# Kernel tuning notes

Measured on AMD Instinct MI355X. Metric: run time of the kernel, lower is better.

Reference implementation:

```python
import jax, jax.numpy as jnp
import numpy as np

N, E, D, C = 100000, 3200000, 256, 47


def _l2norm(x):
    n = jnp.sqrt(jnp.sum(x * x, axis=-1, keepdims=True))
    return x / jnp.maximum(n, 1e-12)


def setup_inputs() -> dict:
    key = jax.random.key(0)
    ks = jax.random.split(key, 12)
    w = lambda k, s: jax.random.normal(k, s, dtype=jnp.float32) * 0.05
    return {
        "x": jax.random.normal(ks[0], (N, D), dtype=jnp.float32),
        "src": jax.random.randint(ks[1], (E,), 0, N, dtype=jnp.int32),
        "dst": jnp.sort(jax.random.randint(ks[2], (E,), 0, N, dtype=jnp.int32)),
        "W_pre": w(ks[3], (D, D)), "b_pre": jnp.zeros((D,), jnp.float32),
        "Wl1": w(ks[4], (D, D)), "bl1": jnp.zeros((D,), jnp.float32),
        "Wr1": w(ks[5], (D, D)),
        "Wl2": w(ks[6], (D, D)), "bl2": jnp.zeros((D,), jnp.float32),
        "Wr2": w(ks[7], (D, D)),
        "W_jk": w(ks[8], (D, D)), "b_jk": jnp.zeros((D,), jnp.float32),
        "W_post": w(ks[9], (C, D)), "b_post": jnp.zeros((C,), jnp.float32),
    }


def _sage_conv(x, src, dst, Wl, bl, Wr):
    # aggr='add': m_i = sum_{j in N(i)} x_j  (SpMM as gather + segment_sum)
    m = jax.ops.segment_sum(x[src], dst, num_segments=N)
    out = m @ Wl.T + bl + x @ Wr.T  # lin_l(aggr) + lin_r(root)
    return _l2norm(out)            # SAGEConv normalize=True


def reference(x, src, dst, W_pre, b_pre, Wl1, bl1, Wr1, Wl2, bl2, Wr2,
              W_jk, b_jk, W_post, b_post):
    # pre-MLP (1 layer) + classifier activation; dropout=0, batch_norm off
    h = jax.nn.relu(x @ W_pre.T + b_pre)
    h = _l2norm(h)  # self.normalize
    # GraphSAGE, jk='last': act+dropout after every conv, then jk lin
    h = jax.nn.relu(_sage_conv(h, src, dst, Wl1, bl1, Wr1))
    h = jax.nn.relu(_sage_conv(h, src, dst, Wl2, bl2, Wr2))
    h = h @ W_jk.T + b_jk
    # post: act + post-MLP (1 layer)
    h = jax.nn.relu(h)
    h = h @ W_post.T + b_post
    return jax.nn.log_softmax(h, axis=-1)
```

## Files before the change

### kernel.cpp

```cpp
#include <hip/hip_runtime.h>
#include <stdint.h>

#define DEV __device__ __forceinline__

typedef __attribute__((ext_vector_type(8))) short bh8;
typedef __attribute__((ext_vector_type(4))) float f4;
#define LDS_AS __attribute__((address_space(3)))
#define GLB_AS __attribute__((address_space(1)))

DEV unsigned short f2bf(float f) {
    union { float f; uint32_t u; } c; c.f = f;
    uint32_t u = c.u;
    uint32_t r = (u + 0x7fffu + ((u >> 16) & 1u)) >> 16;
    return (unsigned short)r;
}
DEV float bf2f(unsigned short h) {
    union { uint32_t u; float f; } c; c.u = ((uint32_t)h) << 16;
    return c.f;
}

DEV uint8_t f2fp8(float v) {
    const float vs = v * 256.f;
    union { float f; uint32_t u; } c; c.f = vs;
    const uint32_t u = c.u + 0x7ffffu + ((c.u >> 20) & 1u);
    const uint32_t f8 = (u >> 20) - 960u;
    return (vs < 0.015625f) ? (uint8_t)0 : (uint8_t)f8;
}
DEV float fp8w(uint32_t x) { union { uint32_t u; float f; } c; c.u = x; return c.f; }

DEV void gload16(const void* g, void* l) {
    __builtin_amdgcn_global_load_lds((const GLB_AS uint32_t*)g, (LDS_AS uint32_t*)l, 16, 0, 0);
}

__global__ __launch_bounds__(256) void prep_kernel(
    const float* __restrict__ x, unsigned short* __restrict__ xb, int n4x, int nbx,
    const float* __restrict__ w0, const float* __restrict__ w1, const float* __restrict__ w2,
    const float* __restrict__ w3, const float* __restrict__ w4, const float* __restrict__ w5,
    unsigned short* __restrict__ wbBase,
    const int* __restrict__ dst, int* __restrict__ rp, int N, int E) {
    const int b = blockIdx.x;
    if (b < nbx) {
        const int i = b * 256 + threadIdx.x;
        if (i < n4x) {
            const float4 v = ((const float4*)x)[i];
            ushort4 o; o.x = f2bf(v.x); o.y = f2bf(v.y); o.z = f2bf(v.z); o.w = f2bf(v.w);
            ((ushort4*)xb)[i] = o;
        }
    } else if (b < nbx + 384) {
        const int wi = (b - nbx) >> 6;
        const int i = ((b - nbx) & 63) * 256 + threadIdx.x;
        const float* s = wi == 0 ? w0 : wi == 1 ? w1 : wi == 2 ? w2 : wi == 3 ? w3 : wi == 4 ? w4 : w5;
        const float4 v = ((const float4*)s)[i];
        ushort4 o; o.x = f2bf(v.x); o.y = f2bf(v.y); o.z = f2bf(v.z); o.w = f2bf(v.w);
        ((ushort4*)(wbBase + (size_t)wi * 65536))[i] = o;
    } else {
        const int i = (b - nbx - 384) * 256 + threadIdx.x;
        if (i <= N) {
            int lo = 0, hi = E;
            while (lo < hi) { int mid = (lo + hi) >> 1; if (dst[mid] < i) lo = mid + 1; else hi = mid; }
            rp[i] = lo;
        }
    }
}

__global__ __launch_bounds__(256) void agg_fp8_kernel(const uint32_t* __restrict__ h32,
                                                      const int* __restrict__ src,
                                                      const int* __restrict__ rp,
                                                      unsigned short* __restrict__ mout, int nNodes) {
    const int node = blockIdx.x * 4 + (threadIdx.x >> 6);
    if (node >= nNodes) return;
    const int lane = threadIdx.x & 63;
    const int beg = __builtin_amdgcn_readfirstlane(rp[node]);
    const int end = __builtin_amdgcn_readfirstlane(rp[node + 1]);
    float a0 = 0.f, a1 = 0.f, a2 = 0.f, a3 = 0.f;
    int e = beg;
    for (; e + 8 <= end; e += 8) {
        int s[8];
#pragma unroll
        for (int i = 0; i < 8; i++) s[i] = src[e + i];
        uint32_t w[8];
#pragma unroll
        for (int i = 0; i < 8; i++) w[i] = h32[(size_t)s[i] * 64 + lane];
#pragma unroll
        for (int i = 0; i < 8; i++) {
            a0 += fp8w((w[i] << 20) & 0x07f00000u);
            a1 += fp8w((w[i] << 12) & 0x07f00000u);
            a2 += fp8w((w[i] << 4)  & 0x07f00000u);
            a3 += fp8w((w[i] >> 4)  & 0x07f00000u);
        }
    }
    for (; e < end; ++e) {
        const uint32_t w = h32[(size_t)src[e] * 64 + lane];
        a0 += fp8w((w << 20) & 0x07f00000u);
        a1 += fp8w((w << 12) & 0x07f00000u);
        a2 += fp8w((w << 4)  & 0x07f00000u);
        a3 += fp8w((w >> 4)  & 0x07f00000u);
    }
    const float sc = 0x1p112f;
    ushort4 o;
    o.x = f2bf(a0 * sc); o.y = f2bf(a1 * sc); o.z = f2bf(a2 * sc); o.w = f2bf(a3 * sc);
    *(ushort4*)&mout[(size_t)node * 256 + (size_t)lane * 4] = o;
}

__global__ __launch_bounds__(256) void agg_kernel(const unsigned short* __restrict__ h,
                                                  const int* __restrict__ src,
                                                  const int* __restrict__ rp,
                                                  unsigned short* __restrict__ mout, int nNodes) {
    const int node = blockIdx.x * 4 + (threadIdx.x >> 6);
    if (node >= nNodes) return;
    const int lane = threadIdx.x & 63;
    const size_t fo = (size_t)lane * 4;
    const int beg = __builtin_amdgcn_readfirstlane(rp[node]);
    const int end = __builtin_amdgcn_readfirstlane(rp[node + 1]);
    float a0 = 0.f, a1 = 0.f, a2 = 0.f, a3 = 0.f;
    int e = beg;
    for (; e + 4 <= end; e += 4) {
        const int s0 = src[e], s1 = src[e+1], s2 = src[e+2], s3 = src[e+3];
        ushort4 v0 = *(const ushort4*)&h[(size_t)s0 * 256 + fo];
        ushort4 v1 = *(const ushort4*)&h[(size_t)s1 * 256 + fo];
        ushort4 v2 = *(const ushort4*)&h[(size_t)s2 * 256 + fo];
        ushort4 v3 = *(const ushort4*)&h[(size_t)s3 * 256 + fo];
        a0 += bf2f(v0.x) + bf2f(v1.x) + bf2f(v2.x) + bf2f(v3.x);
        a1 += bf2f(v0.y) + bf2f(v1.y) + bf2f(v2.y) + bf2f(v3.y);
        a2 += bf2f(v0.z) + bf2f(v1.z) + bf2f(v2.z) + bf2f(v3.z);
        a3 += bf2f(v0.w) + bf2f(v1.w) + bf2f(v2.w) + bf2f(v3.w);
    }
    for (; e < end; ++e) {
        const int s = src[e];
        ushort4 v = *(const ushort4*)&h[(size_t)s * 256 + fo];
        a0 += bf2f(v.x); a1 += bf2f(v.y); a2 += bf2f(v.z); a3 += bf2f(v.w);
    }
    ushort4 o;
    o.x = f2bf(a0); o.y = f2bf(a1); o.z = f2bf(a2); o.w = f2bf(a3);
    *(ushort4*)&mout[(size_t)node * 256 + fo] = o;
}

template <int NSEG, int EPMODE, bool EMIT>
__global__ __launch_bounds__(512) void gemm_kernel(
    const unsigned short* __restrict__ A0, const unsigned short* __restrict__ A1,
    const unsigned short* __restrict__ B0, const unsigned short* __restrict__ B1,
    const float* __restrict__ bias, unsigned short* __restrict__ Out,
    uint8_t* __restrict__ F8, int M) {
    __shared__ unsigned short Alds[2 * 128 * 32];
    __shared__ unsigned short Blds[2 * 256 * 32];
    __shared__ float ssq_lds[8][64];

    const int t = threadIdx.x;
    const int wid = t >> 6;
    const int lane = t & 63;
    const int wr = wid >> 2, wc = wid & 3;
    const int l15 = lane & 15;
    const int kh = lane >> 4;
    const int rowBase = blockIdx.x * 128;

    f4 acc[4][4];
#pragma unroll
    for (int m = 0; m < 4; m++)
#pragma unroll
        for (int n = 0; n < 4; n++) acc[m][n] = f4{0.f, 0.f, 0.f, 0.f};

    const int rA = t >> 2;
    const int sSlotA = (t & 3) ^ ((rA >> 1) & 3);
    int grA = rowBase + rA; if (grA > M - 1) grA = M - 1;
    const size_t gAoff = (size_t)grA * 256 + sSlotA * 8;
    const size_t gBoff0 = (size_t)rA * 256 + sSlotA * 8;
    const size_t gBoff1 = (size_t)(128 + rA) * 256 + sSlotA * 8;

    const int nsteps = NSEG * 8;
    auto STAGE = [&](int s, int buf) {
        const unsigned short* Ap = (NSEG == 2 && s >= 8) ? A1 : A0;
        const unsigned short* Bp = (NSEG == 2 && s >= 8) ? B1 : B0;
        const int k0 = (s & 7) * 32;
        gload16(Ap + gAoff + k0, &Alds[buf * 4096 + wid * 512]);
        gload16(Bp + gBoff0 + k0, &Blds[buf * 8192 + wid * 512]);
        gload16(Bp + gBoff1 + k0, &Blds[buf * 8192 + 4096 + wid * 512]);
    };

    STAGE(0, 0);
    asm volatile("s_waitcnt vmcnt(0)" ::: "memory");
    __syncthreads();

#pragma unroll 2
    for (int s = 0; s < nsteps; ++s) {
        const int cur = s & 1;
        if (s + 1 < nsteps) STAGE(s + 1, cur ^ 1);
        bh8 a[4], b[4];
#pragma unroll
        for (int m = 0; m < 4; m++) {
            const int ra = wr * 64 + m * 16 + l15;
            a[m] = *(const bh8*)&Alds[cur * 4096 + ra * 32 + ((kh ^ ((ra >> 1) & 3)) * 8)];
        }
#pragma unroll
        for (int n = 0; n < 4; n++) {
            const int rb = wc * 64 + n * 16 + l15;
            b[n] = *(const bh8*)&Blds[cur * 8192 + rb * 32 + ((kh ^ ((rb >> 1) & 3)) * 8)];
        }
#pragma unroll
        for (int m = 0; m < 4; m++)
#pragma unroll
            for (int n = 0; n < 4; n++)
                acc[m][n] = __builtin_amdgcn_mfma_f32_16x16x32_bf16(a[m], b[n], acc[m][n], 0, 0, 0);
        asm volatile("s_waitcnt vmcnt(0)" ::: "memory");
        __syncthreads();
    }

    const int cBase = wc * 64 + l15;
    float sq[4][4];
#pragma unroll
    for (int m = 0; m < 4; m++) { sq[m][0] = 0.f; sq[m][1] = 0.f; sq[m][2] = 0.f; sq[m][3] = 0.f; }
#pragma unroll
    for (int n = 0; n < 4; n++) {
        const float bv = bias[cBase + n * 16];
#pragma unroll
        for (int m = 0; m < 4; m++)
#pragma unroll
            for (int r = 0; r < 4; r++) {
                float v = acc[m][n][r] + bv;
                if (EPMODE != 1) v = fmaxf(v, 0.f);
                acc[m][n][r] = v;
                sq[m][r] += v * v;
            }
    }

    if (EPMODE != 2) {
#pragma unroll
        for (int mask = 1; mask < 16; mask <<= 1)
#pragma unroll
            for (int m = 0; m < 4; m++)
#pragma unroll
                for (int r = 0; r < 4; r++) sq[m][r] += __shfl_xor(sq[m][r], mask);
        if (l15 == 0) {
#pragma unroll
            for (int m = 0; m < 4; m++)
#pragma unroll
                for (int r = 0; r < 4; r++) ssq_lds[wid][m * 16 + kh * 4 + r] = sq[m][r];
        }
        __syncthreads();
#pragma unroll
        for (int m = 0; m < 4; m++)
#pragma unroll
            for (int r = 0; r < 4; r++) {
                const int rr = m * 16 + kh * 4 + r;
                const float s = ssq_lds[wr * 4 + 0][rr] + ssq_lds[wr * 4 + 1][rr] +
                                ssq_lds[wr * 4 + 2][rr] + ssq_lds[wr * 4 + 3][rr];
                sq[m][r] = 1.f / fmaxf(sqrtf(s), 1e-12f);
            }
    }

#pragma unroll
    for (int m = 0; m < 4; m++)
#pragma unroll
        for (int r = 0; r < 4; r++) {
            const int grow = rowBase + wr * 64 + m * 16 + kh * 4 + r;
            if (grow < M) {
#pragma unroll
                for (int n = 0; n < 4; n++) {
                    float v = acc[m][n][r];
                    if (EPMODE != 2) v *= sq[m][r];
                    if (EPMODE == 1) v = fmaxf(v, 0.f);
                    Out[(size_t)grow * 256 + cBase + n * 16] = f2bf(v);
                    if (EMIT) F8[(size_t)grow * 256 + cBase + n * 16] = f2fp8(v);
                }
            }
        }
}

__global__ __launch_bounds__(256) void final_kernel(const unsigned short* __restrict__ T,
                                                    const float* __restrict__ Wp,
                                                    const float* __restrict__ bp,
                                                    float* __restrict__ out, int M) {
    __shared__ unsigned short Wlds[48 * 256];
    const int t = threadIdx.x;
    for (int i = t; i < 48 * 32; i += 256) {
        const int rb = i >> 5, slot = i & 31;
        bh8 o;
        if (rb < 47) {
#pragma unroll
            for (int j = 0; j < 8; j++) o[j] = (short)f2bf(Wp[rb * 256 + slot * 8 + j]);
        } else {
#pragma unroll
            for (int j = 0; j < 8; j++) o[j] = 0;
        }
        *(bh8*)&Wlds[rb * 256 + ((slot ^ (rb & 7)) * 8)] = o;
    }
    __syncthreads();
    const int wave = t >> 6, lane = t & 63;
    const int l15 = lane & 15, kh = lane >> 4;
    const int rowBase = blockIdx.x * 64 + wave * 16;
    int gr = rowBase + l15; if (gr > M - 1) gr = M - 1;

    bh8 a[8];
#pragma unroll
    for (int ks = 0; ks < 8; ks++)
        a[ks] = *(const bh8*)&T[(size_t)gr * 256 + ks * 32 + kh * 8];
    f4 acc[3];
#pragma unroll
    for (int n = 0; n < 3; n++) acc[n] = f4{0.f, 0.f, 0.f, 0.f};
#pragma unroll
    for (int ks = 0; ks < 8; ks++)
#pragma unroll
        for (int n = 0; n < 3; n++) {
            const int rb = n * 16 + l15;
            const bh8 b = *(const bh8*)&Wlds[rb * 256 + (((ks * 4 + kh) ^ (rb & 7)) * 8)];
            acc[n] = __builtin_amdgcn_mfma_f32_16x16x32_bf16(a[ks], b, acc[n], 0, 0, 0);
        }

    const int c0 = l15, c1 = 16 + l15, c2 = 32 + l15;
    const float b0 = bp[c0], b1 = bp[c1];
    const float b2 = (l15 < 15) ? bp[c2] : 0.f;
#pragma unroll
    for (int r = 0; r < 4; r++) {
        const int grow = rowBase + kh * 4 + r;
        const float x0 = acc[0][r] + b0;
        const float x1 = acc[1][r] + b1;
        const float x2 = (l15 < 15) ? (acc[2][r] + b2) : -3.0e38f;
        float mx = fmaxf(fmaxf(x0, x1), x2);
#pragma unroll
        for (int msk = 1; msk < 16; msk <<= 1) mx = fmaxf(mx, __shfl_xor(mx, msk));
        float se = __expf(x0 - mx) + __expf(x1 - mx) + ((l15 < 15) ? __expf(x2 - mx) : 0.f);
#pragma unroll
        for (int msk = 1; msk < 16; msk <<= 1) se += __shfl_xor(se, msk);
        const float ls = __logf(se) + mx;
        if (grow < M) {
            float* orow = &out[(size_t)grow * 47];
            orow[c0] = x0 - ls;
            orow[c1] = x1 - ls;
            if (l15 < 15) orow[c2] = x2 - ls;
        }
    }
}

extern "C" void kernel_launch(void* const* d_in, const int* in_sizes, int n_in,
                              void* d_out, int out_size, void* d_ws, size_t ws_size,
                              hipStream_t stream) {
    const float* x      = (const float*)d_in[0];
    const int*   src    = (const int*)d_in[1];
    const int*   dst    = (const int*)d_in[2];
    const float* W_pre  = (const float*)d_in[3];
    const float* b_pre  = (const float*)d_in[4];
    const float* Wl1    = (const float*)d_in[5];
    const float* bl1    = (const float*)d_in[6];
    const float* Wr1    = (const float*)d_in[7];
    const float* Wl2    = (const float*)d_in[8];
    const float* bl2    = (const float*)d_in[9];
    const float* Wr2    = (const float*)d_in[10];
    const float* W_jk   = (const float*)d_in[11];
    const float* b_jk   = (const float*)d_in[12];
    const float* W_post = (const float*)d_in[13];
    const float* b_post = (const float*)d_in[14];

    const int N = in_sizes[0] / 256;
    const int E = in_sizes[1];

    char* ws = (char*)d_ws;
    char* ws0 = ws;
    const size_t HB = (size_t)N * 256 * 2;
    unsigned short* bufA = (unsigned short*)ws; ws += HB;
    unsigned short* bufB = (unsigned short*)ws; ws += HB;
    unsigned short* bufC = (unsigned short*)ws; ws += HB;
    unsigned short* bufD = (unsigned short*)ws; ws += HB;
    unsigned short* wbBase = (unsigned short*)ws; ws += (size_t)6 * 65536 * 2;
    int* rp = (int*)ws; ws += (size_t)(N + 1) * 4;
    uint8_t* f8 = (uint8_t*)ws; ws += (size_t)N * 256;
    const bool useFp8 = ((size_t)(ws - ws0) <= ws_size);

    const int n4x = (N * 256) / 4;
    const int nbx = (n4x + 255) / 256;
    const int nbr = (N + 1 + 255) / 256;
    prep_kernel<<<nbx + 384 + nbr, 256, 0, stream>>>(x, bufA, n4x, nbx,
        W_pre, Wl1, Wr1, Wl2, Wr2, W_jk, wbBase, dst, rp, N, E);
    unsigned short* wb[6];
    for (int i = 0; i < 6; i++) wb[i] = wbBase + (size_t)i * 65536;

    const int gB = (N + 127) / 128;
    const int gAgg = (N + 3) / 4;
    if (useFp8) {
        gemm_kernel<1, 0, true><<<gB, 512, 0, stream>>>(bufA, nullptr, wb[0], nullptr, b_pre, bufB, f8, N);
        agg_fp8_kernel<<<gAgg, 256, 0, stream>>>((const uint32_t*)f8, src, rp, bufC, N);
        gemm_kernel<2, 1, true><<<gB, 512, 0, stream>>>(bufC, bufB, wb[1], wb[2], bl1, bufD, f8, N);
        agg_fp8_kernel<<<gAgg, 256, 0, stream>>>((const uint32_t*)f8, src, rp, bufC, N);
        gemm_kernel<2, 1, false><<<gB, 512, 0, stream>>>(bufC, bufD, wb[3], wb[4], bl2, bufA, nullptr, N);
        gemm_kernel<1, 2, false><<<gB, 512, 0, stream>>>(bufA, nullptr, wb[5], nullptr, b_jk, bufB, nullptr, N);
    } else {
        gemm_kernel<1, 0, false><<<gB, 512, 0, stream>>>(bufA, nullptr, wb[0], nullptr, b_pre, bufB, nullptr, N);
        agg_kernel<<<gAgg, 256, 0, stream>>>(bufB, src, rp, bufC, N);
        gemm_kernel<2, 1, false><<<gB, 512, 0, stream>>>(bufC, bufB, wb[1], wb[2], bl1, bufD, nullptr, N);
        agg_kernel<<<gAgg, 256, 0, stream>>>(bufD, src, rp, bufC, N);
        gemm_kernel<2, 1, false><<<gB, 512, 0, stream>>>(bufC, bufD, wb[3], wb[4], bl2, bufA, nullptr, N);
        gemm_kernel<1, 2, false><<<gB, 512, 0, stream>>>(bufA, nullptr, wb[5], nullptr, b_jk, bufB, nullptr, N);
    }
    final_kernel<<<(N + 63) / 64, 256, 0, stream>>>(bufB, W_post, b_post, (float*)d_out, N);
}
```

Measured before the change: 602.2 us.

## Bucket each node's neighbor list by source range before aggregation

Adds a kernel that reorders each destination's source indices into 16 buckets by the high bits of the source id (8192-node ranges). Both FP8 aggregation passes then read the permuted list, so gathers sweep the feature table in a more local order and should hit cache more often. The sum is unchanged apart from float summation order. The cost is an extra pass over all edges, 16 ballot sweeps per node, and an extra E-sized workspace buffer, and the new path runs only if the workspace is large enough.

```diff
diff --git a/kernel.cpp b/kernel.cpp
--- a/kernel.cpp
+++ b/kernel.cpp
@@ -59,6 +59,29 @@
             int lo = 0, hi = E;
             while (lo < hi) { int mid = (lo + hi) >> 1; if (dst[mid] < i) lo = mid + 1; else hi = mid; }
             rp[i] = lo;
+        }
+    }
+}
+
+__global__ __launch_bounds__(256) void bucket_kernel(const int* __restrict__ src,
+                                                     const int* __restrict__ rp,
+                                                     int* __restrict__ srcp, int nNodes) {
+    const int node = blockIdx.x * 4 + (threadIdx.x >> 6);
+    if (node >= nNodes) return;
+    const int lane = threadIdx.x & 63;
+    const int beg = __builtin_amdgcn_readfirstlane(rp[node]);
+    const int end = __builtin_amdgcn_readfirstlane(rp[node + 1]);
+    int base = beg;
+    for (int p = 0; p < 16; ++p) {
+        for (int c = beg; c < end; c += 64) {
+            const int e = c + lane;
+            const bool valid = e < end;
+            const int s = valid ? src[e] : -1;
+            const bool m = valid && ((s >> 13) == p);
+            const unsigned long long mask = __ballot(m);
+            const int idx = __popcll(mask & ((1ull << lane) - 1ull));
+            if (m) srcp[base + idx] = s;
+            base += __popcll(mask);
         }
     }
 }
@@ -363,6 +386,8 @@
     int* rp = (int*)ws; ws += (size_t)(N + 1) * 4;
     uint8_t* f8 = (uint8_t*)ws; ws += (size_t)N * 256;
     const bool useFp8 = ((size_t)(ws - ws0) <= ws_size);
+    int* srcp = (int*)ws; ws += (size_t)E * 4;
+    const bool useSort = useFp8 && ((size_t)(ws - ws0) <= ws_size);
 
     const int n4x = (N * 256) / 4;
     const int nbx = (n4x + 255) / 256;
@@ -375,10 +400,12 @@
     const int gB = (N + 127) / 128;
     const int gAgg = (N + 3) / 4;
     if (useFp8) {
+        const int* srcUse = useSort ? srcp : src;
+        if (useSort) bucket_kernel<<<gAgg, 256, 0, stream>>>(src, rp, srcp, N);
         gemm_kernel<1, 0, true><<<gB, 512, 0, stream>>>(bufA, nullptr, wb[0], nullptr, b_pre, bufB, f8, N);
-        agg_fp8_kernel<<<gAgg, 256, 0, stream>>>((const uint32_t*)f8, src, rp, bufC, N);
+        agg_fp8_kernel<<<gAgg, 256, 0, stream>>>((const uint32_t*)f8, srcUse, rp, bufC, N);
         gemm_kernel<2, 1, true><<<gB, 512, 0, stream>>>(bufC, bufB, wb[1], wb[2], bl1, bufD, f8, N);
-        agg_fp8_kernel<<<gAgg, 256, 0, stream>>>((const uint32_t*)f8, src, rp, bufC, N);
+        agg_fp8_kernel<<<gAgg, 256, 0, stream>>>((const uint32_t*)f8, srcUse, rp, bufC, N);
         gemm_kernel<2, 1, false><<<gB, 512, 0, stream>>>(bufC, bufD, wb[3], wb[4], bl2, bufA, nullptr, N);
         gemm_kernel<1, 2, false><<<gB, 512, 0, stream>>>(bufA, nullptr, wb[5], nullptr, b_jk, bufB, nullptr, N);
     } else {
```

Measured after the change: 679.6 us. 1.13x slower.

## Fuse input bf16 conversion into first GEMM and JK GEMM into final classifier

Applied to the files above, without the earlier changes.

The separate pass that converts x from fp32 to bf16 is removed, and the first GEMM now reads fp32 x directly, converting it while staging into LDS through registers. The JK linear layer (GEMM plus bias plus ReLU) is merged into the final classifier kernel. Its output tile stays in swizzled LDS and feeds the 47-class projection and log-softmax, so the bf16 intermediate no longer makes a global round trip. The trade-offs are that the first GEMM's A-operand loads move from async global-to-LDS to synchronous register loads at twice the bytes, and the fused kernel uses 64-row tiles with large LDS use per block.

```diff
diff --git a/kernel.cpp b/kernel.cpp
--- a/kernel.cpp
+++ b/kernel.cpp
@@ -33,28 +33,20 @@
 }
 
 __global__ __launch_bounds__(256) void prep_kernel(
-    const float* __restrict__ x, unsigned short* __restrict__ xb, int n4x, int nbx,
     const float* __restrict__ w0, const float* __restrict__ w1, const float* __restrict__ w2,
     const float* __restrict__ w3, const float* __restrict__ w4, const float* __restrict__ w5,
     unsigned short* __restrict__ wbBase,
     const int* __restrict__ dst, int* __restrict__ rp, int N, int E) {
     const int b = blockIdx.x;
-    if (b < nbx) {
-        const int i = b * 256 + threadIdx.x;
-        if (i < n4x) {
-            const float4 v = ((const float4*)x)[i];
-            ushort4 o; o.x = f2bf(v.x); o.y = f2bf(v.y); o.z = f2bf(v.z); o.w = f2bf(v.w);
-            ((ushort4*)xb)[i] = o;
-        }
-    } else if (b < nbx + 384) {
-        const int wi = (b - nbx) >> 6;
-        const int i = ((b - nbx) & 63) * 256 + threadIdx.x;
+    if (b < 384) {
+        const int wi = b >> 6;
+        const int i = (b & 63) * 256 + threadIdx.x;
         const float* s = wi == 0 ? w0 : wi == 1 ? w1 : wi == 2 ? w2 : wi == 3 ? w3 : wi == 4 ? w4 : w5;
         const float4 v = ((const float4*)s)[i];
         ushort4 o; o.x = f2bf(v.x); o.y = f2bf(v.y); o.z = f2bf(v.z); o.w = f2bf(v.w);
         ((ushort4*)(wbBase + (size_t)wi * 65536))[i] = o;
     } else {
-        const int i = (b - nbx - 384) * 256 + threadIdx.x;
+        const int i = (b - 384) * 256 + threadIdx.x;
         if (i <= N) {
             int lo = 0, hi = E;
             while (lo < hi) { int mid = (lo + hi) >> 1; if (dst[mid] < i) lo = mid + 1; else hi = mid; }
@@ -135,15 +127,18 @@
     *(ushort4*)&mout[(size_t)node * 256 + fo] = o;
 }
 
-template <int NSEG, int EPMODE, bool EMIT>
+template <int NSEG, int EPMODE, bool EMIT, bool CVT>
 __global__ __launch_bounds__(512) void gemm_kernel(
-    const unsigned short* __restrict__ A0, const unsigned short* __restrict__ A1,
+    const void* __restrict__ A0v, const unsigned short* __restrict__ A1,
     const unsigned short* __restrict__ B0, const unsigned short* __restrict__ B1,
     const float* __restrict__ bias, unsigned short* __restrict__ Out,
     uint8_t* __restrict__ F8, int M) {
     __shared__ unsigned short Alds[2 * 128 * 32];
     __shared__ unsigned short Blds[2 * 256 * 32];
     __shared__ float ssq_lds[8][64];
+
+    const unsigned short* A0 = (const unsigned short*)A0v;
+    const float* A0f = (const float*)A0v;
 
     const int t = threadIdx.x;
     const int wid = t >> 6;
@@ -168,10 +163,22 @@
 
     const int nsteps = NSEG * 8;
     auto STAGE = [&](int s, int buf) {
-        const unsigned short* Ap = (NSEG == 2 && s >= 8) ? A1 : A0;
         const unsigned short* Bp = (NSEG == 2 && s >= 8) ? B1 : B0;
         const int k0 = (s & 7) * 32;
-        gload16(Ap + gAoff + k0, &Alds[buf * 4096 + wid * 512]);
+        if (CVT) {
+            const float* Af = A0f + gAoff + k0;
+            const float4 v0 = *(const float4*)Af;
+            const float4 v1 = *(const float4*)(Af + 4);
+            bh8 o;
+            o[0] = (short)f2bf(v0.x); o[1] = (short)f2bf(v0.y);
+            o[2] = (short)f2bf(v0.z); o[3] = (short)f2bf(v0.w);
+            o[4] = (short)f2bf(v1.x); o[5] = (short)f2bf(v1.y);
+            o[6] = (short)f2bf(v1.z); o[7] = (short)f2bf(v1.w);
+            *(bh8*)&Alds[buf * 4096 + wid * 512 + lane * 8] = o;
+        } else {
+            const unsigned short* Ap = (NSEG == 2 && s >= 8) ? A1 : A0;
+            gload16(Ap + gAoff + k0, &Alds[buf * 4096 + wid * 512]);
+        }
         gload16(Bp + gBoff0 + k0, &Blds[buf * 8192 + wid * 512]);
         gload16(Bp + gBoff1 + k0, &Blds[buf * 8192 + 4096 + wid * 512]);
     };
@@ -265,12 +272,86 @@
         }
 }
 
-__global__ __launch_bounds__(256) void final_kernel(const unsigned short* __restrict__ T,
-                                                    const float* __restrict__ Wp,
-                                                    const float* __restrict__ bp,
-                                                    float* __restrict__ out, int M) {
-    __shared__ unsigned short Wlds[48 * 256];
+__global__ __launch_bounds__(256) void jkfinal_kernel(
+    const unsigned short* __restrict__ A,
+    const unsigned short* __restrict__ Bjk,
+    const float* __restrict__ bjk,
+    const float* __restrict__ Wp, const float* __restrict__ bp,
+    float* __restrict__ out, int M) {
+    __shared__ unsigned short S[20480];
+    __shared__ unsigned short Tlds[64 * 256];
+
     const int t = threadIdx.x;
+    const int wid = t >> 6;
+    const int lane = t & 63;
+    const int wc = wid;
+    const int l15 = lane & 15;
+    const int kh = lane >> 4;
+    const int rowBase = blockIdx.x * 64;
+
+    f4 acc[4][4];
+#pragma unroll
+    for (int m = 0; m < 4; m++)
+#pragma unroll
+        for (int n = 0; n < 4; n++) acc[m][n] = f4{0.f, 0.f, 0.f, 0.f};
+
+    const int rA = t >> 2;
+    const int sSlotA = (t & 3) ^ ((rA >> 1) & 3);
+    int grA = rowBase + rA; if (grA > M - 1) grA = M - 1;
+    const size_t gAoff = (size_t)grA * 256 + sSlotA * 8;
+    const size_t gBoff = (size_t)rA * 256 + sSlotA * 8;
+
+    auto STAGE = [&](int s, int buf) {
+        const int k0 = s * 32;
+        gload16(A + gAoff + k0, &S[buf * 2048 + wid * 512]);
+#pragma unroll
+        for (int p = 0; p < 4; ++p)
+            gload16(Bjk + (size_t)p * 16384 + gBoff + k0,
+                    &S[4096 + buf * 8192 + p * 2048 + wid * 512]);
+    };
+
+    STAGE(0, 0);
+    asm volatile("s_waitcnt vmcnt(0)" ::: "memory");
+    __syncthreads();
+
+#pragma unroll 2
+    for (int s = 0; s < 8; ++s) {
+        const int cur = s & 1;
+        if (s + 1 < 8) STAGE(s + 1, cur ^ 1);
+        bh8 a[4], b[4];
+#pragma unroll
+        for (int m = 0; m < 4; m++) {
+            const int ra = m * 16 + l15;
+            a[m] = *(const bh8*)&S[cur * 2048 + ra * 32 + ((kh ^ ((ra >> 1) & 3)) * 8)];
+        }
+#pragma unroll
+        for (int n = 0; n < 4; n++) {
+            const int rb = wc * 64 + n * 16 + l15;
+            b[n] = *(const bh8*)&S[4096 + cur * 8192 + rb * 32 + ((kh ^ ((rb >> 1) & 3)) * 8)];
+        }
+#pragma unroll
+        for (int m = 0; m < 4; m++)
+#pragma unroll
+            for (int n = 0; n < 4; n++)
+                acc[m][n] = __builtin_amdgcn_mfma_f32_16x16x32_bf16(a[m], b[n], acc[m][n], 0, 0, 0);
+        asm volatile("s_waitcnt vmcnt(0)" ::: "memory");
+        __syncthreads();
+    }
+
+    const int cBase = wc * 64 + l15;
+#pragma unroll
+    for (int n = 0; n < 4; n++) {
+        const float bv = bjk[cBase + n * 16];
+        const int slot = wc * 4 + n;
+#pragma unroll
+        for (int m = 0; m < 4; m++)
+#pragma unroll
+            for (int r = 0; r < 4; r++) {
+                const int row = m * 16 + kh * 4 + r;
+                const float v = fmaxf(acc[m][n][r] + bv, 0.f);
+                Tlds[row * 256 + (((slot ^ ((row >> 2) & 7)) << 4) | l15)] = f2bf(v);
+            }
+    }
     for (int i = t; i < 48 * 32; i += 256) {
         const int rb = i >> 5, slot = i & 31;
         bh8 o;
@@ -281,28 +362,27 @@
 #pragma unroll
             for (int j = 0; j < 8; j++) o[j] = 0;
         }
-        *(bh8*)&Wlds[rb * 256 + ((slot ^ (rb & 7)) * 8)] = o;
+        *(bh8*)&S[rb * 256 + ((slot ^ (rb & 7)) * 8)] = o;
     }
     __syncthreads();
-    const int wave = t >> 6, lane = t & 63;
-    const int l15 = lane & 15, kh = lane >> 4;
-    const int rowBase = blockIdx.x * 64 + wave * 16;
-    int gr = rowBase + l15; if (gr > M - 1) gr = M - 1;
-
-    bh8 a[8];
-#pragma unroll
-    for (int ks = 0; ks < 8; ks++)
-        a[ks] = *(const bh8*)&T[(size_t)gr * 256 + ks * 32 + kh * 8];
-    f4 acc[3];
-#pragma unroll
-    for (int n = 0; n < 3; n++) acc[n] = f4{0.f, 0.f, 0.f, 0.f};
+
+    const int lrow = wid * 16 + l15;
+    bh8 a2[8];
+#pragma unroll
+    for (int ks = 0; ks < 8; ks++) {
+        const int slot = ks * 2 + (kh >> 1);
+        a2[ks] = *(const bh8*)&Tlds[lrow * 256 + (((slot ^ ((lrow >> 2) & 7)) << 4) | ((kh & 1) * 8))];
+    }
+    f4 acc2[3];
+#pragma unroll
+    for (int n = 0; n < 3; n++) acc2[n] = f4{0.f, 0.f, 0.f, 0.f};
 #pragma unroll
     for (int ks = 0; ks < 8; ks++)
 #pragma unroll
         for (int n = 0; n < 3; n++) {
             const int rb = n * 16 + l15;
-            const bh8 b = *(const bh8*)&Wlds[rb * 256 + (((ks * 4 + kh) ^ (rb & 7)) * 8)];
-            acc[n] = __builtin_amdgcn_mfma_f32_16x16x32_bf16(a[ks], b, acc[n], 0, 0, 0);
+            const bh8 b = *(const bh8*)&S[rb * 256 + (((ks * 4 + kh) ^ (rb & 7)) * 8)];
+            acc2[n] = __builtin_amdgcn_mfma_f32_16x16x32_bf16(a2[ks], b, acc2[n], 0, 0, 0);
         }
 
     const int c0 = l15, c1 = 16 + l15, c2 = 32 + l15;
@@ -310,10 +390,10 @@
     const float b2 = (l15 < 15) ? bp[c2] : 0.f;
 #pragma unroll
     for (int r = 0; r < 4; r++) {
-        const int grow = rowBase + kh * 4 + r;
-        const float x0 = acc[0][r] + b0;
-        const float x1 = acc[1][r] + b1;
-        const float x2 = (l15 < 15) ? (acc[2][r] + b2) : -3.0e38f;
+        const int grow = rowBase + wid * 16 + kh * 4 + r;
+        const float x0 = acc2[0][r] + b0;
+        const float x1 = acc2[1][r] + b1;
+        const float x2 = (l15 < 15) ? (acc2[2][r] + b2) : -3.0e38f;
         float mx = fmaxf(fmaxf(x0, x1), x2);
 #pragma unroll
         for (int msk = 1; msk < 16; msk <<= 1) mx = fmaxf(mx, __shfl_xor(mx, msk));
@@ -364,30 +444,27 @@
     uint8_t* f8 = (uint8_t*)ws; ws += (size_t)N * 256;
     const bool useFp8 = ((size_t)(ws - ws0) <= ws_size);
 
-    const int n4x = (N * 256) / 4;
-    const int nbx = (n4x + 255) / 256;
     const int nbr = (N + 1 + 255) / 256;
-    prep_kernel<<<nbx + 384 + nbr, 256, 0, stream>>>(x, bufA, n4x, nbx,
-        W_pre, Wl1, Wr1, Wl2, Wr2, W_jk, wbBase, dst, rp, N, E);
+    prep_kernel<<<384 + nbr, 256, 0, stream>>>(W_pre, Wl1, Wr1, Wl2, Wr2, W_jk,
+                                               wbBase, dst, rp, N, E);
     unsigned short* wb[6];
     for (int i = 0; i < 6; i++) wb[i] = wbBase + (size_t)i * 65536;
 
     const int gB = (N + 127) / 128;
     const int gAgg = (N + 3) / 4;
     if (useFp8) {
-        gemm_kernel<1, 0, true><<<gB, 512, 0, stream>>>(bufA, nullptr, wb[0], nullptr, b_pre, bufB, f8, N);
+        gemm_kernel<1, 0, true, true><<<gB, 512, 0, stream>>>(x, nullptr, wb[0], nullptr, b_pre, bufB, f8, N);
         agg_fp8_kernel<<<gAgg, 256, 0, stream>>>((const uint32_t*)f8, src, rp, bufC, N);
-        gemm_kernel<2, 1, true><<<gB, 512, 0, stream>>>(bufC, bufB, wb[1], wb[2], bl1, bufD, f8, N);
+        gemm_kernel<2, 1, true, false><<<gB, 512, 0, stream>>>(bufC, bufB, wb[1], wb[2], bl1, bufD, f8, N);
         agg_fp8_kernel<<<gAgg, 256, 0, stream>>>((const uint32_t*)f8, src, rp, bufC, N);
-        gemm_kernel<2, 1, false><<<gB, 512, 0, stream>>>(bufC, bufD, wb[3], wb[4], bl2, bufA, nullptr, N);
-        gemm_kernel<1, 2, false><<<gB, 512, 0, stream>>>(bufA, nullptr, wb[5], nullptr, b_jk, bufB, nullptr, N);
+        gemm_kernel<2, 1, false, false><<<gB, 512, 0, stream>>>(bufC, bufD, wb[3], wb[4], bl2, bufA, nullptr, N);
     } else {
-        gemm_kernel<1, 0, false><<<gB, 512, 0, stream>>>(bufA, nullptr, wb[0], nullptr, b_pre, bufB, nullptr, N);
+        gemm_kernel<1, 0, false, true><<<gB, 512, 0, stream>>>(x, nullptr, wb[0], nullptr, b_pre, bufB, nullptr, N);
         agg_kernel<<<gAgg, 256, 0, stream>>>(bufB, src, rp, bufC, N);
-        gemm_kernel<2, 1, false><<<gB, 512, 0, stream>>>(bufC, bufB, wb[1], wb[2], bl1, bufD, nullptr, N);
+        gemm_kernel<2, 1, false, false><<<gB, 512, 0, stream>>>(bufC, bufB, wb[1], wb[2], bl1, bufD, nullptr, N);
         agg_kernel<<<gAgg, 256, 0, stream>>>(bufD, src, rp, bufC, N);
-        gemm_kernel<2, 1, false><<<gB, 512, 0, stream>>>(bufC, bufD, wb[3], wb[4], bl2, bufA, nullptr, N);
-        gemm_kernel<1, 2, false><<<gB, 512, 0, stream>>>(bufA, nullptr, wb[5], nullptr, b_jk, bufB, nullptr, N);
-    }
-    final_kernel<<<(N + 63) / 64, 256, 0, stream>>>(bufB, W_post, b_post, (float*)d_out, N);
-}
+        gemm_kernel<2, 1, false, false><<<gB, 512, 0, stream>>>(bufC, bufD, wb[3], wb[4], bl2, bufA, nullptr, N);
+    }
+    jkfinal_kernel<<<(N + 63) / 64, 256, 0, stream>>>(bufA, wb[5], b_jk, W_post, b_post,
+                                                      (float*)d_out, N);
+}
```

Measured after the change: 587.3 us. 2.5% less time.
